# Kernel tuning notes

Measured on AMD Instinct MI355X. Metric: run time of the kernel, lower is better.

Reference implementation:

```python
import jax, jax.numpy as jnp
import numpy as np

H = W = 256
L = H * W                      # number of graph vertices / tree leaves
N_NODES = 2 * L - 1            # binary partition tree node count
LAM = 1.0                      # lambda_ (soft-area temperature)


def _grid_edges():
    """4-adjacency grid graph edges (same structure as higra get_4_adjacency_graph)."""
    idx = np.arange(L, dtype=np.int64).reshape(H, W)
    src = np.concatenate([idx[:, :-1].ravel(), idx[:-1, :].ravel()])
    dst = np.concatenate([idx[:, 1:].ravel(), idx[1:, :].ravel()])
    return src.astype(np.int32), dst.astype(np.int32)


def setup_inputs() -> dict:
    key = jax.random.key(0)
    src, dst = _grid_edges()
    ew = jax.random.uniform(key, (src.shape[0],), dtype=jnp.float32)
    return {"edge_weights": ew,
            "edges_src": jnp.asarray(src),
            "edges_dst": jnp.asarray(dst)}


def _build_tree(ew, src, dst):
    """higra.bpt_canonical: Kruskal over stably-sorted edges, building a binary
    merge tree. Leaves are 0..L-1, internal node L+i is created by the i-th MST
    edge. Returns (sizes, mst_edge_map, ancestor paths). All integer structure
    is piecewise-constant w.r.t. edge_weights (no gradient flows through it)."""
    order = np.argsort(ew, kind="stable")
    uf = np.arange(L)

    def find(x):
        r = x
        while uf[r] != r:
            r = uf[r]
        while uf[x] != r:
            uf[x], x = r, uf[x]
        return r

    canon = np.arange(L)                      # tree node of each union-find root
    parent = np.arange(N_NODES)               # self-parent until set (root keeps self)
    sizes = np.ones(N_NODES, dtype=np.float32)
    edge_map = np.zeros(L - 1, dtype=np.int64)
    node = L
    for ei in order:
        a = find(src[ei]); b = find(dst[ei])
        if a == b:
            continue
        na, nb = canon[a], canon[b]
        parent[na] = node
        parent[nb] = node
        sizes[node] = sizes[na] + sizes[nb]
        edge_map[node - L] = ei
        uf[a] = b
        canon[b] = node
        node += 1
    # self-inclusive ancestor paths, padded by repeating the root
    cur = np.arange(N_NODES)
    cols = [cur.copy()]
    while np.any(parent[cur] != cur):
        cur = parent[cur]
        cols.append(cur.copy())
    paths = np.stack(cols, axis=1)            # [N_NODES, D+1]
    return sizes, edge_map, paths


def _softarea(edge_weights, edge_map, sizes_np, paths_np):
    """Soft area of every tree node n:
       area(n) = sum_x sigmoid((alt(n) - d(x, n)) / lambda)
    where d(x,n) is the min ultrametric distance from leaf x to the leaves of n:
      - x in subtree(n), x != n : d = alt(parent(x))
      - x == n (leaf)           : d = 0
      - x outside subtree(n)    : d = alt(lowest ancestor of n containing x).
    Outside leaves are grouped per ancestor a (count = size(a) - size(previous
    node on the path)), giving an O(N * depth) vectorized computation."""
    alt = jnp.concatenate([jnp.zeros((L,), edge_weights.dtype),
                           edge_weights[edge_map]])          # [N_NODES]
    alt_path = alt[paths_np]                                  # [N, D+1]
    size_path = sizes_np[paths_np]                            # constant, numpy
    diff = jnp.asarray(size_path[:, 1:] - size_path[:, :-1])  # 0 on root padding
    outside = jnp.sum(
        diff * jax.nn.sigmoid((alt[:, None] - alt_path[:, 1:]) / LAM), axis=1)

    # inside: each leaf x contributes sigmoid((alt(a_k) - alt(parent(x)))/lam)
    # to every proper ancestor a_k, plus sigmoid(0)=0.5 to itself (alt(leaf)=0).
    lp = paths_np[:L]                                         # [L, D+1]
    alt_lp = alt_path[:L]
    valid = jnp.asarray((lp[:, 1:] != lp[:, :-1]).astype(np.float32))
    vals = jax.nn.sigmoid((alt_lp[:, 1:] - alt_lp[:, 1:2]) / LAM) * valid
    inside = jax.ops.segment_sum(vals.reshape(-1),
                                 jnp.asarray(lp[:, 1:].reshape(-1)),
                                 num_segments=N_NODES)
    inside = inside.at[:L].add(0.5)
    return inside + outside


def reference(edge_weights, edges_src, edges_dst):
    sizes, edge_map, paths = _build_tree(np.asarray(edge_weights),
                                         np.asarray(edges_src),
                                         np.asarray(edges_dst))
    return _softarea(edge_weights, jnp.asarray(edge_map), sizes, paths)
```

## Files before the change

kernel.cpp:

```cpp
#include <hip/hip_runtime.h>
#include <stdint.h>

typedef unsigned int u32;
typedef unsigned short u16;

#define L_VERTS 65536
#define N_EDGES 130560
#define N_NODES 131071
#define NODEPAD 131072

#define CCH 170
#define SCH 768
#define MAXSV 1536
#define HSZ 2048

#define NB 255
#define TPB 64
#define IPT 8
#define IPB 512

__global__ void init_keys(const float* __restrict__ w, u32* __restrict__ keys, u32* __restrict__ vals,
                          u32* szG, u16* canonTop16, u32* parent, float* alt){
  int i = blockIdx.x*blockDim.x + threadIdx.x;
  if(i < N_EDGES){ keys[i] = __float_as_uint(w[i]); vals[i] = (u32)i; }
  if(i < N_NODES){ parent[i]=(u32)i; alt[i]=0.f; }
  if(i < L_VERTS){ szG[i]=1u; canonTop16[i]=0xFFFFu; }
}

__global__ void radix_hist(const u32* __restrict__ idx, const u32* __restrict__ keys,
                           u32* __restrict__ histG, int shift){
  __shared__ u32 h[256];
  for(int i=threadIdx.x;i<256;i+=TPB) h[i]=0;
  __syncthreads();
  int base = blockIdx.x*IPB + threadIdx.x*IPT;
  #pragma unroll
  for(int i=0;i<IPT;i++){
    u32 e = idx[base+i];
    u32 d = (keys[e]>>shift)&255u;
    atomicAdd(&h[d],1u);
  }
  __syncthreads();
  for(int i=threadIdx.x;i<256;i+=TPB) histG[i*NB+blockIdx.x]=h[i];
}

__global__ void radix_scan(u32* histG){
  const int M = 256*NB;
  __shared__ u32 sums[1024];
  int t=threadIdx.x; int s=t*64; u32 acc=0;
  for(int i=0;i<64;i++){int id=s+i; if(id<M) acc+=histG[id];}
  sums[t]=acc; __syncthreads();
  for(int off=1; off<1024; off<<=1){
    u32 v=(t>=off)?sums[t-off]:0u;
    __syncthreads();
    sums[t]+=v;
    __syncthreads();
  }
  u32 run = (t==0)?0u:sums[t-1];
  for(int i=0;i<64;i++){int id=s+i; if(id<M){u32 v=histG[id]; histG[id]=run; run+=v;}}
}

__global__ void radix_scatter(const u32* __restrict__ idxIn, const u32* __restrict__ keys,
                              u32* __restrict__ idxOut, const u32* __restrict__ histG, int shift){
  __shared__ u16 thoff[256][TPB];
  int t=threadIdx.x;
  for(int d=t;d<256;d+=TPB) for(int j=0;j<TPB;j++) thoff[d][j]=0;
  __syncthreads();
  int base = blockIdx.x*IPB + t*IPT;
  u32 myv[IPT]; u32 myd[IPT];
  #pragma unroll
  for(int i=0;i<IPT;i++){
    myv[i]=idxIn[base+i];
    myd[i]=(keys[myv[i]]>>shift)&255u;
    thoff[myd[i]][t]++;
  }
  __syncthreads();
  for(int dd=0;dd<4;dd++){
    int d=t*4+dd; u32 run=0;
    for(int j=0;j<TPB;j++){ u32 v=thoff[d][j]; thoff[d][j]=(u16)run; run+=v; }
  }
  __syncthreads();
  #pragma unroll
  for(int i=0;i<IPT;i++){
    u32 d=myd[i];
    u32 pos = histG[d*NB+blockIdx.x] + (u32)thoff[d][t];
    thoff[d][t]++;
    idxOut[pos]=myv[i];
  }
}

__global__ void build_epair(const u32* __restrict__ order, const int* __restrict__ srcv,
                            const int* __restrict__ dstv, u32* __restrict__ epair){
  int p=blockIdx.x*blockDim.x+threadIdx.x;
  if(p>=N_EDGES) return;
  u32 e=order[p];
  epair[p]=((u32)dstv[e]<<16)|(u32)srcv[e];
}

__device__ __forceinline__ u32 ald(u32* p){
  return __hip_atomic_load(p, __ATOMIC_RELAXED, __HIP_MEMORY_SCOPE_AGENT);
}
__device__ __forceinline__ void ast(u32* p, u32 v){
  __hip_atomic_store(p, v, __ATOMIC_RELAXED, __HIP_MEMORY_SCOPE_AGENT);
}

__global__ void __launch_bounds__(1024,1) p1_checkpoints(
    const u32* __restrict__ epair,
    u32* szG, u16* lid16, u16* svroot16, u16* svsize16, u16* svnext16, u32* mG)
{
  __shared__ u16 ufL[L_VERTS];
  __shared__ u32 hkey[HSZ];
  __shared__ u32 sufL[MAXSV];
  __shared__ u32 compsz[MAXSV];
  __shared__ u32 repkey[MAXSV];
  __shared__ u16 lidL[2*SCH];
  __shared__ u32 mcnt;
  int t = threadIdx.x;
  for(int i=t;i<L_VERTS/2;i+=1024) ((u32*)ufL)[i]=((2u*(u32)i+1u)<<16)|(2u*(u32)i);
  for(int k=0;k<CCH;k++){
    for(int i=t;i<HSZ;i+=1024) hkey[i]=0xFFFFFFFFu;
    for(u32 s=t;s<MAXSV;s+=1024){ sufL[s]=s; compsz[s]=0u; repkey[s]=0u; }
    if(t==0) mcnt=0u;
    __syncthreads();
    int base = k*SCH;
    for(int i=t;i<2*SCH;i+=1024){
      u32 pr = epair[base+(i>>1)];
      u32 v = (i&1)? (pr>>16) : (pr&0xFFFFu);
      u32 x=v;
      while(true){ u32 px=ufL[x]; if(px==x)break; u32 g=ufL[px]; if(g!=px) ufL[x]=(u16)g; x=g; }
      u32 r=x;
      if(v!=r) ufL[v]=(u16)r;
      u32 h=(r*2654435761u)>>21;
      while(true){
        u32 old=atomicCAS(&hkey[h],0xFFFFFFFFu,(r<<16)|0x7FFFu);
        if(old==0xFFFFFFFFu){
          u32 id=atomicAdd(&mcnt,1u);
          svroot16[k*MAXSV+id]=(u16)r;
          hkey[h]=(r<<16)|id;
          break;
        }
        if((old>>16)==r) break;
        h=(h+1)&(HSZ-1u);
      }
      lidL[i]=(u16)h;
    }
    __syncthreads();
    u32 mc=mcnt;
    if(t==0) mG[k]=mc;
    for(u32 s=t;s<mc;s+=1024){
      u32 r=(u32)svroot16[k*MAXSV+s];
      svsize16[k*MAXSV+s]=(u16)(ald(&szG[r])-1u);
    }
    for(int i=t;i<2*SCH;i+=1024) lid16[2*base+i]=(u16)(hkey[lidL[i]]&0xFFFFu);
    for(int j=t;j<SCH;j+=1024){
      u32 sa=hkey[lidL[2*j]]&0xFFFFu, sb=hkey[lidL[2*j+1]]&0xFFFFu;
      if(sa==sb) continue;
      while(true){
        u32 x=sa; while(true){u32 p2=sufL[x]; if(p2==x)break; u32 g=sufL[p2]; if(g!=p2) sufL[x]=g; x=g;}
        u32 y=sb; while(true){u32 p2=sufL[y]; if(p2==y)break; u32 g=sufL[p2]; if(g!=p2) sufL[y]=g; y=g;}
        if(x==y) break;
        u32 hi=x>y?x:y, lo=x^y^hi;
        if(atomicCAS(&sufL[hi],hi,lo)==hi) break;
        sa=hi; sb=lo;
      }
    }
    __syncthreads();
    for(u32 s=t;s<mc;s+=1024){
      u32 x=s; while(true){u32 p2=sufL[x]; if(p2==x)break; x=p2;}
      sufL[s]=x;
      u32 sz=(u32)svsize16[k*MAXSV+s]+1u;
      atomicAdd(&compsz[x], sz);
      atomicMax(&repkey[x], (sz<<11) | (2047u-s));
    }
    __syncthreads();
    for(u32 s=t;s<mc;s+=1024){
      u32 rs=sufL[s];
      u32 rep=2047u-(repkey[rs]&2047u);
      u32 wv=(u32)svroot16[k*MAXSV+rep];
      svnext16[k*MAXSV+s]=(u16)wv;
      u32 myroot=(u32)svroot16[k*MAXSV+s];
      if(myroot!=wv) ufL[myroot]=(u16)wv;
      if(s==rep)     ast(&szG[wv], compsz[rs]);
    }
    __syncthreads();
  }
}

__global__ void __launch_bounds__(64) p2_chunk(
  const u16* __restrict__ lid16,
  const u16* __restrict__ svsize16, const u16* __restrict__ svnext16, const u32* __restrict__ mG,
  u16* __restrict__ outChA, u16* __restrict__ outChB, u16* __restrict__ outSize16, u16* __restrict__ outJ16,
  u32* __restrict__ accCnt, u16* __restrict__ compR16, u16* __restrict__ compTop16, u32* __restrict__ ncomp)
{
  int k = blockIdx.x; int t = threadIdx.x;
  __shared__ u16 uf[MAXSV];
  __shared__ u32 csize[MAXSV];
  __shared__ u16 ctop[MAXSV];
  __shared__ u16 svnl[MAXSV];
  __shared__ u32 lidP[SCH];
  __shared__ u32 cmp_s;
  u32 m = mG[k];
  int base=k*SCH;
  for(u32 s=t;s<m;s+=64){
    uf[s]=(u16)s;
    csize[s]=(u32)svsize16[k*MAXSV+s]+1u;
    ctop[s]=(u16)s;
    svnl[s]=svnext16[k*MAXSV+s];
  }
  for(int j=t;j<SCH;j+=64) lidP[j]=((const u32*)lid16)[base+j];
  if(t==0) cmp_s=0u;
  __syncthreads();
  if(t==0){
    u32 cnt=0;
    for(int j=0;j<SCH;j++){
      u32 lw = lidP[j];
      u32 la = lw & 0xFFFFu, lb = lw >> 16;
      u32 x=la; while(true){u32 px=uf[x]; if(px==x)break; u32 g=uf[px]; uf[x]=(u16)g; x=g;}
      u32 y=lb; while(true){u32 py=uf[y]; if(py==y)break; u32 g=uf[py]; uf[y]=(u16)g; y=g;}
      if(x==y) continue;
      u32 sa=csize[x], sb=csize[y], ns=sa+sb;
      outChA[base+cnt]=ctop[x];
      outChB[base+cnt]=ctop[y];
      outSize16[base+cnt]=(u16)(ns-1u);
      outJ16[base+cnt]=(u16)j;
      u32 win=(sa>=sb)?x:y, los=x^y^win;
      uf[los]=(u16)win; csize[win]=ns; ctop[win]=(u16)(0x8000u|cnt);
      cnt++;
    }
    accCnt[k]=cnt;
  }
  __syncthreads();
  for(u32 s=t;s<m;s+=64){
    if(uf[s]==(u16)s && (ctop[s]&0x8000u)){
      u32 pos=atomicAdd(&cmp_s,1u);
      compR16[k*MAXSV+pos]=svnl[s];
      compTop16[k*MAXSV+pos]=(u16)(ctop[s]&0x7FFFu);
    }
  }
  __syncthreads();
  if(t==0) ncomp[k]=cmp_s;
}

__global__ void __launch_bounds__(1024) p3_stitch(
  const u32* __restrict__ accCnt, const u16* __restrict__ outChA, const u16* __restrict__ outChB,
  const u16* __restrict__ outSize16, const u16* __restrict__ outJ16,
  const u16* __restrict__ svroot16,
  const u16* __restrict__ compR16, const u16* __restrict__ compTop16, const u32* __restrict__ ncomp,
  const u32* __restrict__ order, const float* __restrict__ w,
  u16* __restrict__ canonTop16, u32* __restrict__ parent, float* __restrict__ alt, u16* __restrict__ usize16)
{
  __shared__ u32 accBase[CCH];
  int t=threadIdx.x;
  if(t==0){ u32 r=0; for(int k=0;k<CCH;k++){ accBase[k]=r; r+=accCnt[k]; } }
  __syncthreads();
  for(int idx=t; idx<N_EDGES; idx+=1024){
    int k = idx/SCH; int j = idx - k*SCH;
    if(j < (int)accCnt[k]){
      u32 nid = (u32)L_VERTS + accBase[k] + (u32)j;
      u32 p = (u32)(k*SCH) + (u32)outJ16[idx];
      alt[nid] = w[order[p]];
      usize16[nid] = outSize16[idx];
      u32 cA=outChA[idx]; if(cA & 0x8000u) parent[(u32)L_VERTS+accBase[k]+(cA&0x7FFFu)] = nid;
      u32 cB=outChB[idx]; if(cB & 0x8000u) parent[(u32)L_VERTS+accBase[k]+(cB&0x7FFFu)] = nid;
    }
  }
  __syncthreads();
  for(int k=0;k<CCH;k++){
    u32 ac=accCnt[k];
    for(u32 j=t;j<ac;j+=1024){
      u32 idx=(u32)(k*SCH)+j;
      u32 nid=(u32)L_VERTS+accBase[k]+j;
      u32 cA=outChA[idx];
      if(!(cA&0x8000u)){
        u32 root=(u32)svroot16[k*MAXSV+cA];
        u32 ct=(u32)canonTop16[root];
        parent[(ct==0xFFFFu)?root:((u32)L_VERTS+ct)]=nid;
      }
      u32 cB=outChB[idx];
      if(!(cB&0x8000u)){
        u32 root=(u32)svroot16[k*MAXSV+cB];
        u32 ct=(u32)canonTop16[root];
        parent[(ct==0xFFFFu)?root:((u32)L_VERTS+ct)]=nid;
      }
    }
    __syncthreads();
    u32 nc=ncomp[k];
    for(u32 j=t;j<nc;j+=1024){
      canonTop16[(u32)compR16[k*MAXSV+j]] = (u16)(accBase[k]+compTop16[k*MAXSV+j]);
    }
    __syncthreads();
  }
}

__device__ __forceinline__ void hvals6(float v, float* o){
  float v2=v*v, v3=v2*v, v4=v2*v2, v5=v4*v;
  o[0]=0.5f-0.25f*v+v3*(1.f/48.f)-v5*(1.f/480.f);
  o[1]=0.25f-v2*(1.f/16.f)+v4*(1.f/96.f);
  o[2]=v*(1.f/16.f)-v3*(1.f/48.f);
  o[3]=v2*(1.f/48.f)-(1.f/48.f);
  o[4]=-v*(1.f/96.f);
  o[5]=(1.f/480.f);
}

__global__ void zero_both(u32* cc, float* nodeM, u32* ctr){
  int i=blockIdx.x*blockDim.x+threadIdx.x;
  if(i<L_VERTS) cc[i]=0u;
  if(i<6*NODEPAD) nodeM[i]=0.f;
  if(i==0) *ctr=0u;
}

__global__ void prep_init(const u32* __restrict__ parent, const u16* __restrict__ usize16,
                          u32* cc, u32* J0, uint2* A0, float* out){
  int n=blockIdx.x*blockDim.x+threadIdx.x;
  if(n>=N_NODES) return;
  out[n] = (n<L_VERTS)?0.5f:0.0f;
  if(n==N_NODES-1){ J0[n]=(u32)n; A0[n]=make_uint2(0u,0u); return; }
  u32 p=parent[n];
  u32 ord=atomicAdd(&cc[p-L_VERTS],1u);
  u32 szP=(u32)usize16[p]+1u;
  u32 szN=(n<L_VERTS)?1u:((u32)usize16[n]+1u);
  u32 sib=szP-szN;
  A0[n]=make_uint2(ord? sib:0u, 1u + (ord? (2u*sib-1u):0u));
  J0[n]=p;
}

__global__ void triple_round(const u32* __restrict__ Jin, const uint2* __restrict__ Ain,
                             u32* __restrict__ Jout, uint2* __restrict__ Aout){
  int n=blockIdx.x*blockDim.x+threadIdx.x;
  if(n>=N_NODES) return;
  u32 j1=Jin[n], j2=Jin[j1], j3=Jin[j2], j4=Jin[j3], j5=Jin[j4], j6=Jin[j5], j7=Jin[j6];
  uint2 a0=Ain[n], a1=Ain[j1], a2=Ain[j2], a3=Ain[j3], a4=Ain[j4], a5=Ain[j5], a6=Ain[j6], a7=Ain[j7];
  Aout[n]=make_uint2(a0.x+a1.x+a2.x+a3.x+a4.x+a5.x+a6.x+a7.x,
                     a0.y+a1.y+a2.y+a3.y+a4.y+a5.y+a6.y+a7.y);
  Jout[n]=Jin[j7];
}

__global__ void scatter_all(const u32* __restrict__ parent, const float* __restrict__ alt,
                            const u16* __restrict__ usize16, const uint2* __restrict__ accF,
                            float* __restrict__ leafM, float* __restrict__ nodeM){
  int n=blockIdx.x*blockDim.x+threadIdx.x;
  if(n>=N_NODES) return;
  u32 p=parent[n];
  float h[6]; hvals6(alt[p],h);
  uint2 af=accF[n];
  if(n<L_VERTS){
    u32 pos=af.x;
    #pragma unroll
    for(int j=0;j<6;j++) leafM[(size_t)j*L_VERTS+pos]=h[j];
  }
  if(n<N_NODES-1){
    u32 szP=(u32)usize16[p]+1u;
    u32 szN=(n<L_VERTS)?1u:((u32)usize16[n]+1u);
    float d=(float)(szP-szN);
    u32 q0=af.y;
    u32 q1=q0 + 2u*szN - 1u;
    #pragma unroll
    for(int j=0;j<6;j++){
      float tm=d*h[j];
      atomicAdd(&nodeM[(size_t)j*NODEPAD+q0], tm);
      atomicAdd(&nodeM[(size_t)j*NODEPAD+q1], -tm);
    }
  }
}

__global__ void scanAll(float* __restrict__ leafM, float* __restrict__ nodeM,
                        float* __restrict__ bsumL, float* __restrict__ bsumN, u32* ctr){
  int b=blockIdx.x; int t=threadIdx.x;
  float* arr; u32 base; float* bs;
  if(b<6*64){ int row=b>>6, blk=b&63;  arr=leafM+(size_t)row*L_VERTS;  base=(u32)blk*1024u; bs=&bsumL[row*64+blk]; }
  else      { int bb=b-384; int row=bb>>7, blk=bb&127; arr=nodeM+(size_t)row*NODEPAD; base=(u32)blk*1024u; bs=&bsumN[row*128+blk]; }
  __shared__ float s[256];
  __shared__ u32 lastFlag;
  base += (u32)t*4u;
  float v0=arr[base],v1=arr[base+1],v2=arr[base+2],v3=arr[base+3];
  v1+=v0; v2+=v1; v3+=v2;
  s[t]=v3; __syncthreads();
  for(int o=1;o<256;o<<=1){ float x=(t>=o)?s[t-o]:0.f; __syncthreads(); s[t]+=x; __syncthreads(); }
  float pre=(t>0)?s[t-1]:0.f;
  arr[base]=v0+pre; arr[base+1]=v1+pre; arr[base+2]=v2+pre; arr[base+3]=v3+pre;
  if(t==255) *bs=s[255];
  __threadfence();
  if(t==0) lastFlag = (atomicAdd(ctr,1u)==1151u) ? 1u : 0u;
  __syncthreads();
  if(lastFlag){
    __threadfence();
    if(t<6){ float r=0; for(int i=0;i<64;i++){ float v=bsumL[t*64+i]; bsumL[t*64+i]=r; r+=v; } }
    else if(t<12){ int j=t-6; float r=0; for(int i=0;i<128;i++){ float v=bsumN[j*128+i]; bsumN[j*128+i]=r; r+=v; } }
  }
}

__global__ void eval_all(const uint2* __restrict__ accF, const float* __restrict__ alt,
                         const u16* __restrict__ usize16, const float* __restrict__ leafM,
                         const float* __restrict__ nodeM, const float* __restrict__ bsumL,
                         const float* __restrict__ bsumN, float* __restrict__ out){
  int n=blockIdx.x*blockDim.x+threadIdx.x;
  if(n>=N_NODES) return;
  uint2 af=accF[n];
  float u=alt[n];
  u32 q=af.y;
  float acc=0.f, up=1.f;
  #pragma unroll
  for(int j=0;j<6;j++){
    float T = nodeM[(size_t)j*NODEPAD+q] + bsumN[j*128 + (q>>10)];
    acc += up*T;
    up*=u;
  }
  if(n>=L_VERTS){
    u32 lo=af.x;
    u32 hi=lo + (u32)usize16[n] + 1u;
    up=1.f;
    #pragma unroll
    for(int j=0;j<6;j++){
      const float* arr=leafM + (size_t)j*L_VERTS;
      const float* bs=bsumL + j*64;
      float Ph = arr[hi-1u] + bs[(hi-1u)>>10];
      float Pl = lo ? (arr[lo-1u] + bs[(lo-1u)>>10]) : 0.f;
      acc += up*(Ph-Pl);
      up*=u;
    }
  }
  out[n]+=acc;
}

__global__ void ws_too_small(float* out){
  int i=blockIdx.x*blockDim.x+threadIdx.x;
  if(i<N_NODES) out[i]=1.0e6f;
}

extern "C" void kernel_launch(void* const* d_in, const int* in_sizes, int n_in,
                              void* d_out, int out_size, void* d_ws, size_t ws_size,
                              hipStream_t stream){
  (void)in_sizes; (void)n_in; (void)out_size;
  const float* w  = (const float*)d_in[0];
  const int* src  = (const int*)d_in[1];
  const int* dst  = (const int*)d_in[2];
  float* out = (float*)d_out;

  char* ws = (char*)d_ws;
  size_t off=0;
  auto alloc=[&](size_t bytes)->void*{ void* p = ws+off; off += (bytes+511)&~(size_t)511; return p; };
  u32* parent   =(u32*)alloc((size_t)N_NODES*4);
  float* alt    =(float*)alloc((size_t)N_NODES*4);
  u16* usize16  =(u16*)alloc((size_t)N_NODES*2);
  float* bsumL  =(float*)alloc(6*64*4);
  float* bsumN  =(float*)alloc(6*128*4);
  u32* ctr      =(u32*)alloc(512);
  size_t scratch0=off;
  u32* keys0    =(u32*)alloc((size_t)N_EDGES*4);
  u32* vals0    =(u32*)alloc((size_t)N_EDGES*4);
  u32* vals1    =(u32*)alloc((size_t)N_EDGES*4);
  u32* histG    =(u32*)alloc(256*NB*4);
  u16* canonTop16=(u16*)alloc((size_t)L_VERTS*2);
  u16* outJ16   =(u16*)alloc((size_t)N_EDGES*2);
  u16* svroot16 =(u16*)alloc((size_t)CCH*MAXSV*2);
  u16* svsize16 =(u16*)alloc((size_t)CCH*MAXSV*2);
  u16* svnext16 =(u16*)alloc((size_t)CCH*MAXSV*2);
  u32* mG       =(u32*)alloc(CCH*4);
  u32* accCnt   =(u32*)alloc(CCH*4);
  u32* ncomp    =(u32*)alloc(CCH*4);
  size_t endA=off;
  off=scratch0;
  u32* ccChsum  =(u32*)alloc((size_t)L_VERTS*4);
  u32* J0       =(u32*)alloc((size_t)N_NODES*4);
  u32* J1       =(u32*)alloc((size_t)N_NODES*4);
  uint2* A0     =(uint2*)alloc((size_t)N_NODES*8);
  uint2* A1     =(uint2*)alloc((size_t)N_NODES*8);
  float* nodeM  =(float*)alloc((size_t)6*NODEPAD*4);
  size_t endB=off;
  float* leafM  =(float*)ccChsum;

  if((endA>ws_size)||(endB>ws_size)){
    ws_too_small<<<(N_NODES+255)/256,256,0,stream>>>(out);
    return;
  }

  u16* lid16    =(u16*)vals1;
  u32* epair    =keys0;
  u16* outChA16 =(u16*)histG;
  u16* outChB16 =(u16*)keys0;
  u16* outSize16=(u16*)((char*)keys0 + (size_t)N_EDGES*2);
  u16* compR16  =svsize16;
  u16* compTop16=svnext16;
  u32* szG      =(u32*)usize16;

  init_keys<<<(N_NODES+255)/256,256,0,stream>>>(w,keys0,vals0,szG,canonTop16,parent,alt);
  for(int pass=0;pass<4;pass++){
    const u32* iv = (pass&1)?vals1:vals0;
    u32* ov = (pass&1)?vals0:vals1;
    int shift=pass*8;
    radix_hist   <<<NB,TPB,0,stream>>>(iv,keys0,histG,shift);
    radix_scan   <<<1,1024,0,stream>>>(histG);
    radix_scatter<<<NB,TPB,0,stream>>>(iv,keys0,ov,histG,shift);
  }
  build_epair<<<(N_EDGES+255)/256,256,0,stream>>>(vals0,src,dst,epair);
  p1_checkpoints<<<1,1024,0,stream>>>(epair,szG,lid16,svroot16,svsize16,svnext16,mG);
  p2_chunk<<<CCH,64,0,stream>>>(lid16,svsize16,svnext16,mG,
                                outChA16,outChB16,outSize16,outJ16,accCnt,compR16,compTop16,ncomp);
  p3_stitch<<<1,1024,0,stream>>>(accCnt,outChA16,outChB16,outSize16,outJ16,svroot16,
                                 compR16,compTop16,ncomp,vals0,w,canonTop16,parent,alt,usize16);
  zero_both<<<(6*NODEPAD+255)/256,256,0,stream>>>(ccChsum,nodeM,ctr);
  prep_init<<<(N_NODES+255)/256,256,0,stream>>>(parent,usize16,ccChsum,J1,A1,out);
  for(int r=0;r<6;r++){
    if((r&1)==0) triple_round<<<(N_NODES+255)/256,256,0,stream>>>(J1,A1,J0,A0);
    else         triple_round<<<(N_NODES+255)/256,256,0,stream>>>(J0,A0,J1,A1);
  }
  const uint2* accF=A1;
  scatter_all<<<(N_NODES+255)/256,256,0,stream>>>(parent,alt,usize16,accF,leafM,nodeM);
  scanAll<<<1152,256,0,stream>>>(leafM,nodeM,bsumL,bsumN,ctr);
  eval_all<<<(N_NODES+255)/256,256,0,stream>>>(accF,alt,usize16,leafM,nodeM,bsumL,bsumN,out);
}
```

Measured before the change: 2.923 ms.

## Prefilter MST edges with parallel Boruvka before sequential Kruskal tree build

Adds a parallel Boruvka pass (min-edge by sorted rank, hooking, pointer compression, 16 fixed rounds) that marks the MST edges, then compacts them with a ballot-based scan. The single-block checkpoint and stitch phases then walk only the 65535 MST edges (86 chunks instead of 170). This roughly halves the serial Kruskal work but adds about 64 small kernel launches. It also depends on 16 rounds being enough to reach a spanning tree.

```diff
diff --git a/kernel.cpp b/kernel.cpp
--- a/kernel.cpp
+++ b/kernel.cpp
@@ -3,6 +3,7 @@
 
 typedef unsigned int u32;
 typedef unsigned short u16;
+typedef unsigned long long u64;
 
 #define L_VERTS 65536
 #define N_EDGES 130560
@@ -10,7 +11,10 @@
 #define NODEPAD 131072
 
 #define CCH 170
+#define CCHM 86
 #define SCH 768
+#define PADM (CCHM*SCH)
+#define NMST (L_VERTS-1)
 #define MAXSV 1536
 #define HSZ 2048
 
@@ -94,6 +98,108 @@
   if(p>=N_EDGES) return;
   u32 e=order[p];
   epair[p]=((u32)dstv[e]<<16)|(u32)srcv[e];
+}
+
+#define CBK 255
+#define CT 512
+
+__device__ __forceinline__ u32 bfind(const u32* __restrict__ parentB, u32 x){
+  while(true){ u32 p=parentB[x]; if(p==x) return x; x=p; }
+}
+
+__global__ void bor_init(u32* parentB, u32* minE, unsigned char* mstF){
+  int i=blockIdx.x*blockDim.x+threadIdx.x;
+  if(i<L_VERTS){ parentB[i]=(u32)i; minE[i]=0xFFFFFFFFu; }
+  if(i<N_EDGES) mstF[i]=0;
+}
+
+__global__ void bor_minedge(const u32* __restrict__ epair, const u32* __restrict__ parentB,
+                            u32* __restrict__ minE){
+  int p=blockIdx.x*blockDim.x+threadIdx.x;
+  u32 pr=epair[p];
+  u32 ra=bfind(parentB, pr&0xFFFFu), rb=bfind(parentB, pr>>16);
+  if(ra==rb) return;
+  atomicMin(&minE[ra],(u32)p);
+  atomicMin(&minE[rb],(u32)p);
+}
+
+__global__ void bor_hookA(const u32* __restrict__ epair, const u32* __restrict__ parentB,
+                          const u32* __restrict__ minE, u32* __restrict__ nextB,
+                          unsigned char* __restrict__ mstF){
+  int v=blockIdx.x*blockDim.x+threadIdx.x;
+  if(v>=L_VERTS) return;
+  if(parentB[v]!=(u32)v) return;
+  u32 p=minE[v];
+  if(p==0xFFFFFFFFu) return;
+  u32 pr=epair[p];
+  u32 ra=bfind(parentB, pr&0xFFFFu), rb=bfind(parentB, pr>>16);
+  u32 w2=(ra==(u32)v)?rb:ra;
+  nextB[v]=w2;
+  mstF[p]=1;
+}
+
+__global__ void bor_hookB(u32* __restrict__ parentB, const u32* __restrict__ minE,
+                          const u32* __restrict__ nextB){
+  int v=blockIdx.x*blockDim.x+threadIdx.x;
+  if(v>=L_VERTS) return;
+  if(parentB[v]!=(u32)v) return;
+  u32 p=minE[v];
+  if(p==0xFFFFFFFFu) return;
+  u32 w2=nextB[v];
+  if(minE[w2]==p && (u32)v<w2) return;
+  parentB[v]=w2;
+}
+
+__global__ void bor_compress(u32* __restrict__ parentB, u32* __restrict__ minE){
+  int v=blockIdx.x*blockDim.x+threadIdx.x;
+  if(v>=L_VERTS) return;
+  u32 x=(u32)v;
+  while(true){ u32 px=parentB[x]; if(px==x) break; u32 g=parentB[px]; if(g!=px) parentB[x]=g; x=g; }
+  parentB[v]=x;
+  minE[v]=0xFFFFFFFFu;
+}
+
+__global__ void mst_count(const unsigned char* __restrict__ mstF, u32* __restrict__ blockCnt){
+  int b=blockIdx.x, t=threadIdx.x;
+  int p=b*CT+t;
+  u64 m=__ballot(mstF[p]!=0);
+  __shared__ u32 ws[8];
+  if((t&63)==0) ws[t>>6]=(u32)__popcll(m);
+  __syncthreads();
+  if(t==0){ u32 s=0; for(int i=0;i<8;i++) s+=ws[i]; blockCnt[b]=s; }
+}
+
+__global__ void mst_scan(const u32* __restrict__ blockCnt, u32* __restrict__ blockBase,
+                         u32* __restrict__ mepair){
+  int t=threadIdx.x;
+  __shared__ u32 s[256];
+  u32 v=(t<CBK)?blockCnt[t]:0u;
+  s[t]=v; __syncthreads();
+  for(int o=1;o<256;o<<=1){ u32 x=(t>=o)?s[t-o]:0u; __syncthreads(); s[t]+=x; __syncthreads(); }
+  if(t<CBK) blockBase[t]=s[t]-v;
+  u32 total=s[255];
+  for(u32 j=total+(u32)t; j<(u32)PADM; j+=256u) mepair[j]=0u;
+}
+
+__global__ void mst_scatter(const unsigned char* __restrict__ mstF, const u32* __restrict__ blockBase,
+                            const u32* __restrict__ order, const u32* __restrict__ epair,
+                            u32* __restrict__ morder, u32* __restrict__ mepair){
+  int b=blockIdx.x, t=threadIdx.x;
+  int p=b*CT+t;
+  u32 f=(u32)mstF[p];
+  u64 m=__ballot(f!=0);
+  __shared__ u32 ws[8];
+  int wid=t>>6, lane=t&63;
+  if(lane==0) ws[wid]=(u32)__popcll(m);
+  __syncthreads();
+  if(t==0){ u32 s2=0; for(int i=0;i<8;i++){ u32 x=ws[i]; ws[i]=s2; s2+=x; } }
+  __syncthreads();
+  if(f){
+    u32 pre=(u32)__popcll(m & ((1ull<<lane)-1ull));
+    u32 pos=blockBase[b]+ws[wid]+pre;
+    morder[pos]=order[p];
+    mepair[pos]=epair[p];
+  }
 }
 
 __device__ __forceinline__ u32 ald(u32* p){
@@ -116,7 +222,7 @@
   __shared__ u32 mcnt;
   int t = threadIdx.x;
   for(int i=t;i<L_VERTS/2;i+=1024) ((u32*)ufL)[i]=((2u*(u32)i+1u)<<16)|(2u*(u32)i);
-  for(int k=0;k<CCH;k++){
+  for(int k=0;k<CCHM;k++){
     for(int i=t;i<HSZ;i+=1024) hkey[i]=0xFFFFFFFFu;
     for(u32 s=t;s<MAXSV;s+=1024){ sufL[s]=s; compsz[s]=0u; repkey[s]=0u; }
     if(t==0) mcnt=0u;
@@ -245,26 +351,26 @@
   const u16* __restrict__ outSize16, const u16* __restrict__ outJ16,
   const u16* __restrict__ svroot16,
   const u16* __restrict__ compR16, const u16* __restrict__ compTop16, const u32* __restrict__ ncomp,
-  const u32* __restrict__ order, const float* __restrict__ w,
+  const u32* __restrict__ morder, const float* __restrict__ w,
   u16* __restrict__ canonTop16, u32* __restrict__ parent, float* __restrict__ alt, u16* __restrict__ usize16)
 {
   __shared__ u32 accBase[CCH];
   int t=threadIdx.x;
-  if(t==0){ u32 r=0; for(int k=0;k<CCH;k++){ accBase[k]=r; r+=accCnt[k]; } }
-  __syncthreads();
-  for(int idx=t; idx<N_EDGES; idx+=1024){
+  if(t==0){ u32 r=0; for(int k=0;k<CCHM;k++){ accBase[k]=r; r+=accCnt[k]; } }
+  __syncthreads();
+  for(int idx=t; idx<PADM; idx+=1024){
     int k = idx/SCH; int j = idx - k*SCH;
     if(j < (int)accCnt[k]){
       u32 nid = (u32)L_VERTS + accBase[k] + (u32)j;
       u32 p = (u32)(k*SCH) + (u32)outJ16[idx];
-      alt[nid] = w[order[p]];
+      alt[nid] = w[morder[p]];
       usize16[nid] = outSize16[idx];
       u32 cA=outChA[idx]; if(cA & 0x8000u) parent[(u32)L_VERTS+accBase[k]+(cA&0x7FFFu)] = nid;
       u32 cB=outChB[idx]; if(cB & 0x8000u) parent[(u32)L_VERTS+accBase[k]+(cB&0x7FFFu)] = nid;
     }
   }
   __syncthreads();
-  for(int k=0;k<CCH;k++){
+  for(int k=0;k<CCHM;k++){
     u32 ac=accCnt[k];
     for(u32 j=t;j<ac;j+=1024){
       u32 idx=(u32)(k*SCH)+j;
@@ -457,6 +563,14 @@
   u32* mG       =(u32*)alloc(CCH*4);
   u32* accCnt   =(u32*)alloc(CCH*4);
   u32* ncomp    =(u32*)alloc(CCH*4);
+  u32* parentB  =(u32*)alloc((size_t)L_VERTS*4);
+  u32* minE     =(u32*)alloc((size_t)L_VERTS*4);
+  u32* nextB    =(u32*)alloc((size_t)L_VERTS*4);
+  unsigned char* mstF=(unsigned char*)alloc((size_t)N_EDGES);
+  u32* blockCnt =(u32*)alloc(256*4);
+  u32* blockBase=(u32*)alloc(256*4);
+  u32* morder   =(u32*)alloc((size_t)PADM*4);
+  u32* mepair   =(u32*)alloc((size_t)PADM*4);
   size_t endA=off;
   off=scratch0;
   u32* ccChsum  =(u32*)alloc((size_t)L_VERTS*4);
@@ -492,11 +606,21 @@
     radix_scatter<<<NB,TPB,0,stream>>>(iv,keys0,ov,histG,shift);
   }
   build_epair<<<(N_EDGES+255)/256,256,0,stream>>>(vals0,src,dst,epair);
-  p1_checkpoints<<<1,1024,0,stream>>>(epair,szG,lid16,svroot16,svsize16,svnext16,mG);
-  p2_chunk<<<CCH,64,0,stream>>>(lid16,svsize16,svnext16,mG,
+  bor_init<<<CBK,CT,0,stream>>>(parentB,minE,mstF);
+  for(int r=0;r<16;r++){
+    bor_minedge <<<CBK,CT,0,stream>>>(epair,parentB,minE);
+    bor_hookA   <<<L_VERTS/CT,CT,0,stream>>>(epair,parentB,minE,nextB,mstF);
+    bor_hookB   <<<L_VERTS/CT,CT,0,stream>>>(parentB,minE,nextB);
+    bor_compress<<<L_VERTS/CT,CT,0,stream>>>(parentB,minE);
+  }
+  mst_count  <<<CBK,CT,0,stream>>>(mstF,blockCnt);
+  mst_scan   <<<1,256,0,stream>>>(blockCnt,blockBase,mepair);
+  mst_scatter<<<CBK,CT,0,stream>>>(mstF,blockBase,vals0,epair,morder,mepair);
+  p1_checkpoints<<<1,1024,0,stream>>>(mepair,szG,lid16,svroot16,svsize16,svnext16,mG);
+  p2_chunk<<<CCHM,64,0,stream>>>(lid16,svsize16,svnext16,mG,
                                 outChA16,outChB16,outSize16,outJ16,accCnt,compR16,compTop16,ncomp);
   p3_stitch<<<1,1024,0,stream>>>(accCnt,outChA16,outChB16,outSize16,outJ16,svroot16,
-                                 compR16,compTop16,ncomp,vals0,w,canonTop16,parent,alt,usize16);
+                                 compR16,compTop16,ncomp,morder,w,canonTop16,parent,alt,usize16);
   zero_both<<<(6*NODEPAD+255)/256,256,0,stream>>>(ccChsum,nodeM,ctr);
   prep_init<<<(N_NODES+255)/256,256,0,stream>>>(parent,usize16,ccChsum,J1,A1,out);
   for(int r=0;r<6;r++){
```

Result: faster. 2.699 ms (-7.7%).
